# Kernel optimization log

Hardware: AMD Instinct MI355X
Metric: run time of the kernel (lower is better)

Reference implementation:

```python
import jax, jax.numpy as jnp
import numpy as np
import math

DIM = 1536
N_HEADS = 12
HEAD_DIM = DIM // N_HEADS  # 128
C = HEAD_DIM // 2          # 64 complex rotation channels
CT = C - 2 * (C // 3)      # 22 temporal channels
CH = C // 3                # 21 height channels
CW = C // 3                # 21 width channels
F, H, W = 3, 30, 52        # video latent grid -> S = 4680
S = F * H * W
B = 1
EPS = 1e-6
NEG = -1e30


def _rope_angles(max_pos, sizes):
    # Wan-style rope_params per axis: theta_j = 10000^(-j/m) for m complex dims
    parts = []
    pos = jnp.arange(max_pos, dtype=jnp.float32)
    for m in sizes:
        inv = 10000.0 ** (-jnp.arange(m, dtype=jnp.float32) / m)
        parts.append(pos[:, None] * inv[None, :])
    return jnp.concatenate(parts, axis=-1)  # [max_pos, C]


def setup_inputs() -> dict:
    key = jax.random.key(0)
    ks = jax.random.split(key, 6)
    sc = 0.02
    inp = {
        'x': jax.random.normal(ks[0], (B, S, DIM), jnp.float32),
        'seq_lens': jnp.array([S], dtype=jnp.int32),
        'grid_sizes': jnp.array([[F, H, W]], dtype=jnp.int32),
        'freqs': _rope_angles(1024, [CT, CH, CW]),  # [1024, 64] rotation angles
        'Wq': jax.random.normal(ks[1], (DIM, DIM), jnp.float32) * sc,
        'bq': jnp.zeros((DIM,), jnp.float32),
        'Wk': jax.random.normal(ks[2], (DIM, DIM), jnp.float32) * sc,
        'bk': jnp.zeros((DIM,), jnp.float32),
        'Wv': jax.random.normal(ks[3], (DIM, DIM), jnp.float32) * sc,
        'bv': jnp.zeros((DIM,), jnp.float32),
        'Wo': jax.random.normal(ks[4], (DIM, DIM), jnp.float32) * sc,
        'bo': jnp.zeros((DIM,), jnp.float32),
        'gq': jnp.ones((DIM,), jnp.float32),
        'gk': jnp.ones((DIM,), jnp.float32),
    }
    return inp


def _rmsnorm(x, g):
    return x * jax.lax.rsqrt(jnp.mean(x * x, axis=-1, keepdims=True) + EPS) * g


def _apply_rope(x, grid_sizes, freqs):
    # x: [B, S, n, d]; rotate consecutive pairs by 3D (t,h,w) factorized angles.
    b, s, n, d = x.shape
    f = grid_sizes[0, 0]
    h = grid_sizes[0, 1]
    w = grid_sizes[0, 2]
    pos = jnp.arange(s)
    t_idx = pos // (h * w)
    y_idx = (pos % (h * w)) // w
    x_idx = pos % w
    ang = jnp.concatenate([
        freqs[t_idx, :CT],
        freqs[y_idx, CT:CT + CH],
        freqs[x_idx, CT + CH:],
    ], axis=-1)  # [S, C]
    cos = jnp.cos(ang)[None, :, None, :]  # [1, S, 1, C]
    sin = jnp.sin(ang)[None, :, None, :]
    xp = x.reshape(b, s, n, d // 2, 2)
    xr, xi = xp[..., 0], xp[..., 1]
    out_r = xr * cos - xi * sin
    out_i = xr * sin + xi * cos
    return jnp.stack([out_r, out_i], axis=-1).reshape(b, s, n, d)


def reference(x, seq_lens, grid_sizes, freqs, Wq, bq, Wk, bk, Wv, bv, Wo, bo, gq, gk):
    b, s, _ = x.shape
    n, d = N_HEADS, HEAD_DIM
    q = _rmsnorm(x @ Wq.T + bq, gq).reshape(b, s, n, d)
    k = _rmsnorm(x @ Wk.T + bk, gk).reshape(b, s, n, d)
    v = (x @ Wv.T + bv).reshape(b, s, n, d)

    rq = _apply_rope(q, grid_sizes, freqs)
    rk = _apply_rope(k, grid_sizes, freqs)

    # frame-level block-causal mask (block_mask in the original flex_attention)
    frame_seqlen = grid_sizes[0, 1] * grid_sizes[0, 2]
    frame_id = jnp.arange(s) // frame_seqlen
    allowed = frame_id[:, None] >= frame_id[None, :]  # [S, S]

    scale = 1.0 / math.sqrt(d)
    scores = jnp.einsum('bqnd,bknd->bnqk', rq, rk) * scale
    scores = jnp.where(allowed[None, None], scores, NEG)
    attn = jax.nn.softmax(scores, axis=-1)
    out = jnp.einsum('bnqk,bknd->bqnd', attn, v).reshape(b, s, n * d)
    return out @ Wo.T + bo
```

## Files before the change

### kernel.cpp

```cpp
#include <hip/hip_runtime.h>
#include <hip/hip_bf16.h>
#include <math.h>
#include <stdint.h>

#define S_LEN 4680
#define DIMSZ 1536
#define NH    12
#define HD    128
#define FRAME 1560
#define NGRP  74
#define PANH  (NGRP * 8192)
#define NSLOT 150

typedef _Float16 f16;
typedef _Float16 f16x8 __attribute__((ext_vector_type(8)));
typedef _Float16 f16x4 __attribute__((ext_vector_type(4)));
typedef _Float16 f16x2 __attribute__((ext_vector_type(2)));
typedef __fp16   fp16x2 __attribute__((ext_vector_type(2)));
typedef float    f32x4  __attribute__((ext_vector_type(4)));
typedef float    f32x16 __attribute__((ext_vector_type(16)));
typedef int      v2i    __attribute__((ext_vector_type(2)));

__device__ __forceinline__ void async16(const void* g, void* l) {
    __builtin_amdgcn_global_load_lds((const __attribute__((address_space(1))) void*)g,
                                     (__attribute__((address_space(3))) void*)l, 16, 0, 0);
}

union PkCast { fp16x2 v; int i; };
union FragCast { int w[4]; f16x8 v; };

__global__ __launch_bounds__(256) void cast_all(const float* __restrict__ x,
                                                const float* __restrict__ wq,
                                                const float* __restrict__ wk,
                                                const float* __restrict__ wv,
                                                const float* __restrict__ wo,
                                                f16* __restrict__ xh,
                                                f16* __restrict__ wh) {
    int y = blockIdx.y;
    int i = blockIdx.x * 256 + threadIdx.x;
    if (y == 0) {
        if (i < (S_LEN * DIMSZ) / 4) {
            float4 v = ((const float4*)x)[i];
            f16x4 h; h[0]=(f16)v.x; h[1]=(f16)v.y; h[2]=(f16)v.z; h[3]=(f16)v.w;
            ((f16x4*)xh)[i] = h;
        }
    } else {
        const int nW4 = (DIMSZ * DIMSZ) / 4;
        if (i < nW4) {
            const float* src = (y==1)?wq:(y==2)?wk:(y==3)?wv:wo;
            float4 v = ((const float4*)src)[i];
            f16x4 h; h[0]=(f16)v.x; h[1]=(f16)v.y; h[2]=(f16)v.z; h[3]=(f16)v.w;
            ((f16x4*)wh)[(size_t)(y-1)*nW4 + i] = h;
        }
    }
}

__global__ __launch_bounds__(256) void gemm_qkv(const f16* __restrict__ A,
                                                const f16* __restrict__ Bq,
                                                const f16* __restrict__ Bk,
                                                const f16* __restrict__ Bv,
                                                const float* __restrict__ bq,
                                                const float* __restrict__ bk,
                                                const float* __restrict__ bv,
                                                f16* __restrict__ preq,
                                                f16* __restrict__ prek,
                                                f16* __restrict__ vtp) {
    int z = blockIdx.z;
    const f16* B = (z==0) ? Bq : (z==1) ? Bk : Bv;
    const float* bias = (z==0) ? bq : (z==1) ? bk : bv;

    __shared__ __align__(16) f16 Al[128 * 64];
    __shared__ __align__(16) f16 Bl[128 * 64];
    int tid = threadIdx.x;
    int lane = tid & 63, wv = tid >> 6;
    int l16 = lane & 15, quad = lane >> 4;
    int wr = (wv >> 1) * 64, wc = (wv & 1) * 64;
    int m0 = blockIdx.x * 128, n0 = blockIdx.y * 128;

    f32x4 acc[4][4] = {};

    for (int kb = 0; kb < DIMSZ; kb += 64) {
        __syncthreads();
#pragma unroll
        for (int j = 0; j < 4; j++) {
            int s = j * 256 + wv * 64 + lane;
            int r = s >> 3, cc = s & 7;
            const f16* src = A + (size_t)min(m0 + r, S_LEN - 1) * DIMSZ + kb + ((cc ^ (r & 7)) << 3);
            async16(src, (char*)Al + (j * 4096 + wv * 1024));
        }
#pragma unroll
        for (int j = 0; j < 4; j++) {
            int s = j * 256 + wv * 64 + lane;
            int r = s >> 3, cc = s & 7;
            const f16* src = B + (size_t)(n0 + r) * DIMSZ + kb + ((cc ^ (r & 7)) << 3);
            async16(src, (char*)Bl + (j * 4096 + wv * 1024));
        }
        __builtin_amdgcn_s_waitcnt(0x0f70);
        __syncthreads();

#pragma unroll
        for (int kc = 0; kc < 2; kc++) {
            f16x8 af[4], bf[4];
#pragma unroll
            for (int i = 0; i < 4; i++) {
                int ar = wr + i * 16 + l16;
                af[i] = *(const f16x8*)((const char*)Al + ar * 128 + (((kc * 4 + quad) ^ (ar & 7)) << 4));
                int br = wc + i * 16 + l16;
                bf[i] = *(const f16x8*)((const char*)Bl + br * 128 + (((kc * 4 + quad) ^ (br & 7)) << 4));
            }
#pragma unroll
            for (int mi = 0; mi < 4; mi++)
#pragma unroll
                for (int ni = 0; ni < 4; ni++)
                    acc[mi][ni] = __builtin_amdgcn_mfma_f32_16x16x32_f16(af[mi], bf[ni], acc[mi][ni], 0, 0, 0);
        }
    }

    if (z < 2) {
        f16* C = (z == 0) ? preq : prek;
#pragma unroll
        for (int mi = 0; mi < 4; mi++)
#pragma unroll
            for (int ni = 0; ni < 4; ni++) {
                int col = n0 + wc + ni * 16 + l16;
                float bv_ = bias[col];
#pragma unroll
                for (int r = 0; r < 4; r++) {
                    int row = m0 + wr + mi * 16 + quad * 4 + r;
                    if (row < S_LEN) C[(size_t)row * DIMSZ + col] = (f16)(acc[mi][ni][r] + bv_);
                }
            }
    } else {
#pragma unroll
        for (int mi = 0; mi < 4; mi++)
#pragma unroll
            for (int ni = 0; ni < 4; ni++) {
                int col  = n0 + wc + ni * 16 + l16;
                int vhead = col >> 7, d = col & 127;
                int base = m0 + wr + mi * 16 + quad * 4;
                if (base < S_LEN) {
                    float bv_ = bias[col];
                    f16x4 h;
#pragma unroll
                    for (int r = 0; r < 4; r++) h[r] = (f16)(acc[mi][ni][r] + bv_);
                    size_t off = (size_t)vhead * PANH + (size_t)(base >> 6) * 8192
                               + ((base >> 3) & 7) * 1024 + d * 8 + (base & 7);
                    *(f16x4*)(vtp + off) = h;
                }
            }
    }
}

__global__ __launch_bounds__(256) void norm_rope(const f16* __restrict__ preq,
                                                 const f16* __restrict__ prek,
                                                 const float* __restrict__ gq,
                                                 const float* __restrict__ gk,
                                                 const float* __restrict__ freqs,
                                                 f16* __restrict__ Qp,
                                                 f16* __restrict__ Kp) {
    int s = blockIdx.x, which = blockIdx.y;
    int t = threadIdx.x;
    const f16* pre = which ? prek : preq;
    const float* g = which ? gk : gq;
    f16* dst = which ? Kp : Qp;
    const f16* row = pre + (size_t)s * DIMSZ + t * 6;

    float v[6];
    float ss = 0.f;
#pragma unroll
    for (int i = 0; i < 3; i++) {
        f16x2 hp = *(const f16x2*)(row + 2 * i);
        v[2*i] = (float)hp[0]; v[2*i+1] = (float)hp[1];
        ss += v[2*i]*v[2*i] + v[2*i+1]*v[2*i+1];
    }
#pragma unroll
    for (int off = 32; off; off >>= 1) ss += __shfl_xor(ss, off);
    __shared__ float red[4];
    if ((t & 63) == 0) red[t >> 6] = ss;
    __syncthreads();
    float tot = red[0] + red[1] + red[2] + red[3];
    float rms = rsqrtf(tot * (1.0f / DIMSZ) + 1e-6f);

    int tpos = s / FRAME;
    int rem  = s % FRAME;
    int ypos = rem / 52;
    int xpos = s % 52;

#pragma unroll
    for (int u = 0; u < 3; u++) {
        int c = t * 6 + u * 2;
        int head = c >> 7;
        int d = c & 127;
        int j = d >> 1;
        int idx = (j < 22) ? tpos : ((j < 43) ? ypos : xpos);
        float ang = freqs[idx * 64 + j];
        float sn, cs;
        __sincosf(ang, &sn, &cs);
        float vr = v[u * 2]     * rms * g[c];
        float vi = v[u * 2 + 1] * rms * g[c + 1];
        f16* o = dst + (size_t)head * PANH + (size_t)(s >> 6) * 8192
               + (d >> 3) * 512 + (s & 63) * 8 + (d & 7);
        o[0] = (f16)(vr * cs - vi * sn);
        o[1] = (f16)(vr * sn + vi * cs);
    }
}

__global__ __launch_bounds__(128, 2) void attn_part(const f16* __restrict__ Qp,
                                                    const f16* __restrict__ Kp,
                                                    const f16* __restrict__ Vp,
                                                    f16* __restrict__ Opart,
                                                    float* __restrict__ lpart) {
    int bx = blockIdx.x, head = blockIdx.y;
    int t, c, NC2;
    if (bx < 24)      { t = bx >> 1;             c = bx & 1;       NC2 = 2; }
    else if (bx < 72) { t = 12 + ((bx - 24) >> 2); c = (bx - 24) & 3; NC2 = 4; }
    else              { t = 24 + (bx - 72) / 6;  c = (bx - 72) % 6; NC2 = 6; }

    int qlast = min(t * 128 + 127, S_LEN - 1);
    int nfrm  = qlast / FRAME + 1;
    int kvend = nfrm * FRAME; if (kvend > S_LEN) kvend = S_LEN;
    int nG    = (kvend + 63) >> 6;
    int g0 = (c * nG) / NC2, g1 = ((c + 1) * nG) / NC2;
    int limB = ((t * 128) / FRAME + 1) * FRAME;

    int tid = threadIdx.x, lane = tid & 63, wv = tid >> 6;
    int l31 = lane & 31, lh = lane >> 5;
    int qw = t * 128 + wv * 64;

    __shared__ __align__(16) char smem[65536];

    const f16* Qg = Qp + ((size_t)head * NGRP + (qw >> 6)) * 8192;
    f16x8 bqf[2][8];
#pragma unroll
    for (int nt = 0; nt < 2; nt++)
#pragma unroll
        for (int ks = 0; ks < 8; ks++) {
            f16x8 vq = *(const f16x8*)(Qg + (2 * ks + lh) * 512 + (l31 + 32 * nt) * 8);
            bqf[nt][ks] = vq * (f16)0.08838834764831845f;
        }

    int lim[2];
#pragma unroll
    for (int nt = 0; nt < 2; nt++) {
        int q = qw + l31 + 32 * nt;
        lim[nt] = (q / FRAME + 1) * FRAME;
    }

    f32x16 oacc[4][2] = {};
    float lp[2] = {0.f, 0.f};

    int koff = lh * 1024 + l31 * 16;
    int voff = lh * 2048 + l31 * 16;

    const f16* Kh = Kp + (size_t)head * NGRP * 8192;
    const f16* Vh = Vp + (size_t)head * NGRP * 8192;

#pragma unroll
    for (int i = 0; i < 8; i++) {
        int s = i * 2 + wv;
        async16(Kh + (size_t)g0 * 8192 + s * 512 + lane * 8,
                (char*)smem + s * 1024 + lane * 16);
        async16(Vh + (size_t)g0 * 8192 + s * 512 + lane * 8,
                (char*)smem + 16384 + s * 1024 + lane * 16);
    }

    int cur = 0;
    for (int g = g0; g < g1; g++) {
        int kb = g * 64;

        if (g + 1 < g1) {
            int nb = (cur ^ 1) << 15;
#pragma unroll
            for (int i = 0; i < 8; i++) {
                int s = i * 2 + wv;
                async16(Kh + (size_t)(g + 1) * 8192 + s * 512 + lane * 8,
                        (char*)smem + nb + s * 1024 + lane * 16);
                async16(Vh + (size_t)(g + 1) * 8192 + s * 512 + lane * 8,
                        (char*)smem + nb + 16384 + s * 1024 + lane * 16);
            }
            asm volatile("s_waitcnt vmcnt(16)" ::: "memory");
        } else {
            asm volatile("s_waitcnt vmcnt(0)" ::: "memory");
        }
        __builtin_amdgcn_s_barrier();

        const char* smc = (const char*)smem + (cur << 15);
        bool domask = (kb + 64 > limB);

#pragma unroll
        for (int kt = 0; kt < 2; kt++) {
            f32x16 sc0 = {}, sc1 = {};
#pragma unroll
            for (int h = 0; h < 2; h++) {
                f16x8 ka[4];
#pragma unroll
                for (int i = 0; i < 4; i++)
                    ka[i] = *(const f16x8*)(smc + koff + (h * 4 + i) * 2048 + kt * 512);
#pragma unroll
                for (int i = 0; i < 4; i++) {
                    sc0 = __builtin_amdgcn_mfma_f32_32x32x16_f16(ka[i], bqf[0][h*4+i], sc0, 0, 0, 0);
                    sc1 = __builtin_amdgcn_mfma_f32_32x32x16_f16(ka[i], bqf[1][h*4+i], sc1, 0, 0, 0);
                }
            }

            int w[2][8];
            int keyb = kb + kt * 32 + 4 * lh;
#pragma unroll
            for (int nt = 0; nt < 2; nt++) {
#pragma unroll
                for (int p = 0; p < 8; p++) {
                    const int r0 = 2 * p;
                    float s0 = (nt == 0) ? sc0[r0]     : sc1[r0];
                    float s1 = (nt == 0) ? sc0[r0 + 1] : sc1[r0 + 1];
                    if (domask) {
                        int k0 = keyb + (r0 & 3) + 8 * (r0 >> 2);
                        if (k0     >= lim[nt]) s0 = -1e30f;
                        if (k0 + 1 >= lim[nt]) s1 = -1e30f;
                    }
                    float p0 = __expf(s0), p1 = __expf(s1);
                    lp[nt] += p0 + p1;
                    PkCast pk; pk.v = __builtin_amdgcn_cvt_pkrtz(p0, p1);
                    w[nt][p] = pk.i;
                }
            }

            f16x8 pb[2][2];
#pragma unroll
            for (int nt = 0; nt < 2; nt++)
#pragma unroll
                for (int ks = 0; ks < 2; ks++) {
                    FragCast fc;
#if __has_builtin(__builtin_amdgcn_permlane32_swap)
                    v2i r02 = __builtin_amdgcn_permlane32_swap(w[nt][4*ks+0], w[nt][4*ks+2], false, false);
                    v2i r13 = __builtin_amdgcn_permlane32_swap(w[nt][4*ks+1], w[nt][4*ks+3], false, false);
                    fc.w[0] = r02.x; fc.w[1] = r13.x; fc.w[2] = r02.y; fc.w[3] = r13.y;
#else
                    int w0 = w[nt][4*ks], w1 = w[nt][4*ks+1], w2 = w[nt][4*ks+2], w3 = w[nt][4*ks+3];
                    fc.w[0] = lh ? __shfl_xor(w2, 32) : w0;
                    fc.w[1] = lh ? __shfl_xor(w3, 32) : w1;
                    fc.w[2] = lh ? w2 : __shfl_xor(w0, 32);
                    fc.w[3] = lh ? w3 : __shfl_xor(w1, 32);
#endif
                    pb[nt][ks] = fc.v;
                }

#pragma unroll
            for (int mt = 0; mt < 4; mt++)
#pragma unroll
                for (int ks = 0; ks < 2; ks++) {
                    f16x8 va = *(const f16x8*)(smc + 16384 + voff + kt * 8192 + ks * 4096 + mt * 512);
                    oacc[mt][0] = __builtin_amdgcn_mfma_f32_32x32x16_f16(va, pb[0][ks], oacc[mt][0], 0, 0, 0);
                    oacc[mt][1] = __builtin_amdgcn_mfma_f32_32x32x16_f16(va, pb[1][ks], oacc[mt][1], 0, 0, 0);
                }
        }

        __builtin_amdgcn_s_barrier();
        cur ^= 1;
    }

    float lt[2], linv[2];
#pragma unroll
    for (int nt = 0; nt < 2; nt++) {
        float l = lp[nt] + __shfl_xor(lp[nt], 32);
        lt[nt] = l;
        linv[nt] = (l > 0.f) ? 1.f / l : 0.f;
    }

    __syncthreads();
    char* ob = (char*)smem + wv * 16384;
#pragma unroll
    for (int mt = 0; mt < 4; mt++)
#pragma unroll
        for (int nt = 0; nt < 2; nt++) {
            int qloc = l31 + 32 * nt;
#pragma unroll
            for (int g4 = 0; g4 < 4; g4++) {
                f16x4 hv;
#pragma unroll
                for (int r = 0; r < 4; r++) hv[r] = (f16)(oacc[mt][nt][g4 * 4 + r] * linv[nt]);
                int c16 = g4 + 4 * mt;
                *(f16x4*)(ob + qloc * 256 + ((c16 ^ (qloc & 7)) << 4) + lh * 8) = hv;
            }
        }
    __syncthreads();

    size_t obase = ((size_t)(head * NSLOT + bx) * 128 + wv * 64) * HD;
#pragma unroll
    for (int a = 0; a < 4; a++)
#pragma unroll
        for (int b = 0; b < 4; b++) {
            int qloc = a * 16 + (lane >> 2);
            int c16  = (lane & 3) + 4 * b;
            f16x8 vv = *(const f16x8*)(ob + qloc * 256 + ((c16 ^ (qloc & 7)) << 4));
            *(f16x8*)(Opart + obase + (size_t)qloc * HD + c16 * 8) = vv;
        }

    if (lane < 32) {
        size_t lbase = (size_t)(head * NSLOT + bx) * 128 + wv * 64;
        lpart[lbase + l31]      = lt[0];
        lpart[lbase + l31 + 32] = lt[1];
    }
}

__global__ __launch_bounds__(256) void combine(const f16* __restrict__ Opart,
                                               const float* __restrict__ lpart,
                                               f16* __restrict__ AO) {
    int gid = blockIdx.x * 256 + threadIdx.x;
    if (gid >= S_LEN * NH * 16) return;
    int dc = gid & 15;
    int head = (gid >> 4) % NH;
    int q = gid / (NH * 16);
    int tt = q >> 7, qloc = q & 127;
    int base, nchunk;
    if (tt < 12)      { base = 2 * tt;             nchunk = 2; }
    else if (tt < 24) { base = 24 + 4 * (tt - 12); nchunk = 4; }
    else              { base = 72 + 6 * (tt - 24); nchunk = 6; }

    float sum[8] = {};
    float ls = 0.f;
    for (int c = 0; c < nchunk; c++) {
        size_t sbase = (size_t)(head * NSLOT + base + c) * 128 + qloc;
        float l = lpart[sbase];
        if (l > 0.f) {
            f16x8 o = *(const f16x8*)(Opart + sbase * HD + dc * 8);
#pragma unroll
            for (int j = 0; j < 8; j++) sum[j] += (float)o[j] * l;
            ls += l;
        }
    }
    float invl = 1.f / ls;
    f16x8 r;
#pragma unroll
    for (int j = 0; j < 8; j++) r[j] = (f16)(sum[j] * invl);
    *(f16x8*)(AO + (size_t)q * DIMSZ + head * HD + dc * 8) = r;
}

__global__ __launch_bounds__(256) void gemm_lds(const f16* __restrict__ A,
                                                const f16* __restrict__ B,
                                                const float* __restrict__ bias,
                                                float* __restrict__ C) {
    __shared__ __align__(16) f16 Al[128 * 64];
    __shared__ __align__(16) f16 Bl[128 * 64];
    int tid = threadIdx.x;
    int lane = tid & 63, wv = tid >> 6;
    int l16 = lane & 15, quad = lane >> 4;
    int wr = (wv >> 1) * 64, wc = (wv & 1) * 64;
    int m0 = blockIdx.x * 128, n0 = blockIdx.y * 128;

    f32x4 acc[4][4] = {};

    for (int kb = 0; kb < DIMSZ; kb += 64) {
        __syncthreads();
#pragma unroll
        for (int j = 0; j < 4; j++) {
            int s = j * 256 + wv * 64 + lane;
            int r = s >> 3, cc = s & 7;
            const f16* src = A + (size_t)min(m0 + r, S_LEN - 1) * DIMSZ + kb + ((cc ^ (r & 7)) << 3);
            async16(src, (char*)Al + (j * 4096 + wv * 1024));
        }
#pragma unroll
        for (int j = 0; j < 4; j++) {
            int s = j * 256 + wv * 64 + lane;
            int r = s >> 3, cc = s & 7;
            const f16* src = B + (size_t)(n0 + r) * DIMSZ + kb + ((cc ^ (r & 7)) << 3);
            async16(src, (char*)Bl + (j * 4096 + wv * 1024));
        }
        __builtin_amdgcn_s_waitcnt(0x0f70);
        __syncthreads();

#pragma unroll
        for (int kc = 0; kc < 2; kc++) {
            f16x8 af[4], bf[4];
#pragma unroll
            for (int i = 0; i < 4; i++) {
                int ar = wr + i * 16 + l16;
                af[i] = *(const f16x8*)((const char*)Al + ar * 128 + (((kc * 4 + quad) ^ (ar & 7)) << 4));
                int br = wc + i * 16 + l16;
                bf[i] = *(const f16x8*)((const char*)Bl + br * 128 + (((kc * 4 + quad) ^ (br & 7)) << 4));
            }
#pragma unroll
            for (int mi = 0; mi < 4; mi++)
#pragma unroll
                for (int ni = 0; ni < 4; ni++)
                    acc[mi][ni] = __builtin_amdgcn_mfma_f32_16x16x32_f16(af[mi], bf[ni], acc[mi][ni], 0, 0, 0);
        }
    }

#pragma unroll
    for (int mi = 0; mi < 4; mi++)
#pragma unroll
        for (int ni = 0; ni < 4; ni++) {
            int col = n0 + wc + ni * 16 + l16;
            float bv = bias[col];
#pragma unroll
            for (int r = 0; r < 4; r++) {
                int row = m0 + wr + mi * 16 + quad * 4 + r;
                if (row < S_LEN) C[(size_t)row * DIMSZ + col] = acc[mi][ni][r] + bv;
            }
        }
}

extern "C" void kernel_launch(void* const* d_in, const int* in_sizes, int n_in,
                              void* d_out, int out_size, void* d_ws, size_t ws_size,
                              hipStream_t stream) {
    const float* x     = (const float*)d_in[0];
    const float* freqs = (const float*)d_in[3];
    const float* Wq = (const float*)d_in[4];
    const float* bq = (const float*)d_in[5];
    const float* Wk = (const float*)d_in[6];
    const float* bk = (const float*)d_in[7];
    const float* Wv = (const float*)d_in[8];
    const float* bv = (const float*)d_in[9];
    const float* Wo = (const float*)d_in[10];
    const float* bo = (const float*)d_in[11];
    const float* gq = (const float*)d_in[12];
    const float* gk = (const float*)d_in[13];
    float* out = (float*)d_out;

    char* ws = (char*)d_ws;
    const size_t SZ_XH  = (size_t)S_LEN * DIMSZ * 2;
    const size_t SZ_W   = (size_t)DIMSZ * DIMSZ * 2;
    const size_t SZ_PAN = (size_t)NH * PANH * 2;
    const size_t SZ_OP  = (size_t)NH * NSLOT * 128 * HD * 2;

    size_t off = 0;
    f16* xh   = (f16*)(ws + off); off += SZ_XH;
    f16* wqh  = (f16*)(ws + off); off += 4 * SZ_W;
    f16* wkh  = wqh + (size_t)DIMSZ * DIMSZ;
    f16* wvh  = wkh + (size_t)DIMSZ * DIMSZ;
    f16* woh  = wvh + (size_t)DIMSZ * DIMSZ;
    f16* Qpan = (f16*)(ws + off); off += SZ_PAN;
    f16* Kpan = (f16*)(ws + off); off += SZ_PAN;
    f16* Vpan = (f16*)(ws + off); off += SZ_PAN;
    f16* AO   = (f16*)(ws + off); off += SZ_XH;
    f16*   preq  = (f16*)(ws + off);
    f16*   prek  = preq + (size_t)S_LEN * DIMSZ;
    f16*   Opart = (f16*)(ws + off);
    float* lpart = (float*)(ws + off + SZ_OP);

    cast_all<<<dim3(7020, 5), 256, 0, stream>>>(x, Wq, Wk, Wv, Wo, xh, wqh);

    gemm_qkv<<<dim3(37, 12, 3), 256, 0, stream>>>(xh, wqh, wkh, wvh, bq, bk, bv,
                                                  preq, prek, Vpan);

    norm_rope<<<dim3(S_LEN, 2), 256, 0, stream>>>(preq, prek, gq, gk, freqs, Qpan, Kpan);

    attn_part<<<dim3(NSLOT, 12), 128, 0, stream>>>(Qpan, Kpan, Vpan, Opart, lpart);
    combine<<<(S_LEN * NH * 16 + 255) / 256, 256, 0, stream>>>(Opart, lpart, AO);

    gemm_lds<<<dim3(37, 12), 256, 0, stream>>>(AO, woh, bo, out);
}
```

Baseline: 476.6 us.

## Stream V from global into registers, use exp2 with folded scale, set MFMA priority

In the attention kernel, the V tile is no longer staged through LDS. Each lane loads its V fragments straight from global memory into registers at the top of each key block, before the QK^T MFMAs, and only K stays double-buffered through LDS. This halves the shared memory allocation, which may allow more resident blocks, and drops the LDS reads for V, at the cost of more registers and exposed global-load latency. The exp is replaced by hardware exp2 with log2(e) folded into the Q pre-scale, s_setprio is raised around the MFMA sections, and the attention-output buffer now aliases the Q panel workspace.

```diff
diff --git a/kernel.cpp b/kernel.cpp
--- a/kernel.cpp
+++ b/kernel.cpp
@@ -24,6 +24,14 @@
 __device__ __forceinline__ void async16(const void* g, void* l) {
     __builtin_amdgcn_global_load_lds((const __attribute__((address_space(1))) void*)g,
                                      (__attribute__((address_space(3))) void*)l, 16, 0, 0);
+}
+
+__device__ __forceinline__ float fexp2(float x) {
+#if __has_builtin(__builtin_amdgcn_exp2f)
+    return __builtin_amdgcn_exp2f(x);
+#else
+    return exp2f(x);
+#endif
 }
 
 union PkCast { fp16x2 v; int i; };
@@ -227,7 +235,7 @@
     int l31 = lane & 31, lh = lane >> 5;
     int qw = t * 128 + wv * 64;
 
-    __shared__ __align__(16) char smem[65536];
+    __shared__ __align__(16) char smem[32768];
 
     const f16* Qg = Qp + ((size_t)head * NGRP + (qw >> 6)) * 8192;
     f16x8 bqf[2][8];
@@ -236,7 +244,7 @@
 #pragma unroll
         for (int ks = 0; ks < 8; ks++) {
             f16x8 vq = *(const f16x8*)(Qg + (2 * ks + lh) * 512 + (l31 + 32 * nt) * 8);
-            bqf[nt][ks] = vq * (f16)0.08838834764831845f;
+            bqf[nt][ks] = vq * (f16)0.12752044581f;
         }
 
     int lim[2];
@@ -250,46 +258,53 @@
     float lp[2] = {0.f, 0.f};
 
     int koff = lh * 1024 + l31 * 16;
-    int voff = lh * 2048 + l31 * 16;
 
     const f16* Kh = Kp + (size_t)head * NGRP * 8192;
     const f16* Vh = Vp + (size_t)head * NGRP * 8192;
+    const f16* Vl = Vh + lh * 1024 + l31 * 8;
 
 #pragma unroll
     for (int i = 0; i < 8; i++) {
         int s = i * 2 + wv;
         async16(Kh + (size_t)g0 * 8192 + s * 512 + lane * 8,
                 (char*)smem + s * 1024 + lane * 16);
-        async16(Vh + (size_t)g0 * 8192 + s * 512 + lane * 8,
-                (char*)smem + 16384 + s * 1024 + lane * 16);
     }
 
     int cur = 0;
     for (int g = g0; g < g1; g++) {
         int kb = g * 64;
 
+        const f16* Vg = Vl + (size_t)g * 8192;
+        f16x8 va[2][8];
+#pragma unroll
+        for (int kt = 0; kt < 2; kt++)
+#pragma unroll
+            for (int mt = 0; mt < 4; mt++)
+#pragma unroll
+                for (int ks = 0; ks < 2; ks++)
+                    va[kt][mt * 2 + ks] = *(const f16x8*)(Vg + kt * 4096 + ks * 2048 + mt * 256);
+
         if (g + 1 < g1) {
-            int nb = (cur ^ 1) << 15;
+            int nb = (cur ^ 1) << 14;
 #pragma unroll
             for (int i = 0; i < 8; i++) {
                 int s = i * 2 + wv;
                 async16(Kh + (size_t)(g + 1) * 8192 + s * 512 + lane * 8,
                         (char*)smem + nb + s * 1024 + lane * 16);
-                async16(Vh + (size_t)(g + 1) * 8192 + s * 512 + lane * 8,
-                        (char*)smem + nb + 16384 + s * 1024 + lane * 16);
-            }
+            }
+            asm volatile("s_waitcnt vmcnt(24)" ::: "memory");
+        } else {
             asm volatile("s_waitcnt vmcnt(16)" ::: "memory");
-        } else {
-            asm volatile("s_waitcnt vmcnt(0)" ::: "memory");
         }
         __builtin_amdgcn_s_barrier();
 
-        const char* smc = (const char*)smem + (cur << 15);
+        const char* smc = (const char*)smem + (cur << 14);
         bool domask = (kb + 64 > limB);
 
 #pragma unroll
         for (int kt = 0; kt < 2; kt++) {
             f32x16 sc0 = {}, sc1 = {};
+            __builtin_amdgcn_s_setprio(1);
 #pragma unroll
             for (int h = 0; h < 2; h++) {
                 f16x8 ka[4];
@@ -302,6 +317,7 @@
                     sc1 = __builtin_amdgcn_mfma_f32_32x32x16_f16(ka[i], bqf[1][h*4+i], sc1, 0, 0, 0);
                 }
             }
+            __builtin_amdgcn_s_setprio(0);
 
             int w[2][8];
             int keyb = kb + kt * 32 + 4 * lh;
@@ -317,7 +333,7 @@
                         if (k0     >= lim[nt]) s0 = -1e30f;
                         if (k0 + 1 >= lim[nt]) s1 = -1e30f;
                     }
-                    float p0 = __expf(s0), p1 = __expf(s1);
+                    float p0 = fexp2(s0), p1 = fexp2(s1);
                     lp[nt] += p0 + p1;
                     PkCast pk; pk.v = __builtin_amdgcn_cvt_pkrtz(p0, p1);
                     w[nt][p] = pk.i;
@@ -344,14 +360,16 @@
                     pb[nt][ks] = fc.v;
                 }
 
+            __builtin_amdgcn_s_setprio(1);
 #pragma unroll
             for (int mt = 0; mt < 4; mt++)
 #pragma unroll
                 for (int ks = 0; ks < 2; ks++) {
-                    f16x8 va = *(const f16x8*)(smc + 16384 + voff + kt * 8192 + ks * 4096 + mt * 512);
-                    oacc[mt][0] = __builtin_amdgcn_mfma_f32_32x32x16_f16(va, pb[0][ks], oacc[mt][0], 0, 0, 0);
-                    oacc[mt][1] = __builtin_amdgcn_mfma_f32_32x32x16_f16(va, pb[1][ks], oacc[mt][1], 0, 0, 0);
+                    f16x8 vaf = va[kt][mt * 2 + ks];
+                    oacc[mt][0] = __builtin_amdgcn_mfma_f32_32x32x16_f16(vaf, pb[0][ks], oacc[mt][0], 0, 0, 0);
+                    oacc[mt][1] = __builtin_amdgcn_mfma_f32_32x32x16_f16(vaf, pb[1][ks], oacc[mt][1], 0, 0, 0);
                 }
+            __builtin_amdgcn_s_setprio(0);
         }
 
         __builtin_amdgcn_s_barrier();
@@ -532,7 +550,7 @@
     f16* Qpan = (f16*)(ws + off); off += SZ_PAN;
     f16* Kpan = (f16*)(ws + off); off += SZ_PAN;
     f16* Vpan = (f16*)(ws + off); off += SZ_PAN;
-    f16* AO   = (f16*)(ws + off); off += SZ_XH;
+    f16* AO   = Qpan;
     f16*   preq  = (f16*)(ws + off);
     f16*   prek  = preq + (size_t)S_LEN * DIMSZ;
     f16*   Opart = (f16*)(ws + off);
```

Result: slower. 729.0 us (+53.0%).
